# Kernel optimization log

Hardware: AMD Instinct MI355X
Metric: run time of the kernel (lower is better)

The kernel has to match this reference:

```python
import jax, jax.numpy as jnp
import numpy as np

HIDDEN = 4096
MOE_INTER = 1024
SHARED_INTER = 4096  # intermediate_size * num_shared_expert
NUM_EXPERTS = 16
TOP_K = 2


def setup_inputs() -> dict:
    key = jax.random.key(0)
    ks = jax.random.split(key, 6)
    s = 0.02
    hidden_states = jax.random.normal(ks[0], (2, 2048, HIDDEN), dtype=jnp.float32)
    gate_w = jax.random.normal(ks[1], (NUM_EXPERTS, HIDDEN), dtype=jnp.float32) * s
    # per-expert SwiGLU weights: gate_up [E, 2I, H], down [E, H, I]
    w_gate_up = jax.random.normal(ks[2], (NUM_EXPERTS, 2 * MOE_INTER, HIDDEN), dtype=jnp.float32) * s
    w_down = jax.random.normal(ks[3], (NUM_EXPERTS, HIDDEN, MOE_INTER), dtype=jnp.float32) * s
    shared_w_gate_up = jax.random.normal(ks[4], (2 * SHARED_INTER, HIDDEN), dtype=jnp.float32) * s
    shared_w_down = jax.random.normal(ks[5], (HIDDEN, SHARED_INTER), dtype=jnp.float32) * s
    return {
        'hidden_states': hidden_states,
        'gate_w': gate_w,
        'w_gate_up': w_gate_up,
        'w_down': w_down,
        'shared_w_gate_up': shared_w_gate_up,
        'shared_w_down': shared_w_down,
    }


def _moe_forward(x, gate_w, w_gate_up, w_down, shared_w_gate_up, shared_w_down):
    orig_shape = x.shape
    x2 = x.reshape(-1, orig_shape[-1])  # [T, H]

    # shared SwiGLU MLP (reduce_results=False in TP; single device here)
    gu_s = x2 @ shared_w_gate_up.T  # [T, 2*Is]
    g_s, u_s = jnp.split(gu_s, 2, axis=-1)
    shared_out = (jax.nn.silu(g_s) * u_s) @ shared_w_down.T  # [T, H]

    # router: softmax -> top-k -> renormalize (top_k > 1)
    logits = x2 @ gate_w.T  # [T, E]
    probs = jax.nn.softmax(logits, axis=-1)
    topk_vals, topk_idx = jax.lax.top_k(probs, TOP_K)  # [T, K]
    topk_vals = topk_vals / jnp.sum(topk_vals, axis=-1, keepdims=True)
    # combine weights [T, E]: sparse top-k weights scattered into dense matrix
    combine = jnp.sum(
        jax.nn.one_hot(topk_idx, NUM_EXPERTS, dtype=x2.dtype) * topk_vals[..., None],
        axis=1,
    )

    # dense per-expert SwiGLU (reference for fused grouped-GEMM)
    gu = jnp.einsum('th,eih->eti', x2, w_gate_up)  # [E, T, 2I]
    g, u = jnp.split(gu, 2, axis=-1)
    act = jax.nn.silu(g) * u  # [E, T, I]
    out_e = jnp.einsum('eti,ehi->eth', act, w_down)  # [E, T, H]
    moe_out = jnp.einsum('eth,te->th', out_e, combine)  # [T, H]

    return (moe_out + shared_out).reshape(orig_shape)


def reference(hidden_states, gate_w, w_gate_up, w_down, shared_w_gate_up, shared_w_down):
    return _moe_forward(hidden_states, gate_w, w_gate_up, w_down,
                        shared_w_gate_up, shared_w_down)
```

## Files before the change

### kernel.cpp

```cpp
#include <hip/hip_runtime.h>
#include <hip/hip_bf16.h>

#define H 4096
#define MOE_I 1024
#define SH_I 4096
#define NE 16
#define T_TOK 4096
#define NPAIR 8192

using bf16x8 = __attribute__((ext_vector_type(8))) short;
using f32x4  = __attribute__((ext_vector_type(4))) float;

__device__ __forceinline__ unsigned short f2bf(float f) {
    unsigned int x = __float_as_uint(f);
    x += 0x7fffu + ((x >> 16) & 1u);
    return (unsigned short)(x >> 16);
}
__device__ __forceinline__ float bf2f(unsigned short u) {
    return __uint_as_float(((unsigned int)u) << 16);
}

__device__ __forceinline__ void gld_lds16(const void* g, void* l) {
    __builtin_amdgcn_global_load_lds(
        (const __attribute__((address_space(1))) void*)g,
        (__attribute__((address_space(3))) void*)l, 16, 0, 0);
}

__global__ __launch_bounds__(256)
void cast_kernel(const float4* __restrict__ src, ushort4* __restrict__ dst, int n4) {
    int i = blockIdx.x * 256 + threadIdx.x;
    if (i < n4) {
        float4 f = src[i];
        ushort4 o;
        o.x = f2bf(f.x); o.y = f2bf(f.y); o.z = f2bf(f.z); o.w = f2bf(f.w);
        dst[i] = o;
    }
}

__global__ __launch_bounds__(256)
void router_kernel(const float* __restrict__ x, const float* __restrict__ gw,
                   int* __restrict__ topk_id, float* __restrict__ topk_w,
                   int* __restrict__ counts) {
    int t = blockIdx.x;
    const float* xr = x + (size_t)t * H;
    __shared__ float lg[NE];
    int tid = threadIdx.x, w = tid >> 6, lane = tid & 63;
#pragma unroll
    for (int i = 0; i < 4; i++) {
        int e = w * 4 + i;
        const float* g = gw + (size_t)e * H;
        float s = 0.f;
        for (int k = lane; k < H; k += 64) s += xr[k] * g[k];
#pragma unroll
        for (int m = 32; m > 0; m >>= 1) s += __shfl_xor(s, m, 64);
        if (lane == 0) lg[e] = s;
    }
    __syncthreads();
    if (tid == 0) {
        int e0 = 0; float l0 = lg[0];
        for (int e = 1; e < NE; e++) if (lg[e] > l0) { l0 = lg[e]; e0 = e; }
        int e1 = -1; float l1 = -1e30f;
        for (int e = 0; e < NE; e++) if (e != e0 && lg[e] > l1) { l1 = lg[e]; e1 = e; }
        float w1 = 1.f / (1.f + __expf(l0 - l1));
        topk_id[2*t] = e0; topk_id[2*t+1] = e1;
        topk_w[2*t] = 1.f - w1; topk_w[2*t+1] = w1;
        atomicAdd(&counts[e0], 1); atomicAdd(&counts[e1], 1);
    }
}

__global__ void scan16(const int* __restrict__ counts, int* __restrict__ offsets,
                       int* __restrict__ cursor) {
    if (threadIdx.x == 0 && blockIdx.x == 0) {
        int s = 0;
        for (int e = 0; e < NE; e++) { offsets[e] = s; cursor[e] = s; s += counts[e]; }
        offsets[NE] = s;
    }
}

__global__ __launch_bounds__(256)
void assign_kernel(const int* __restrict__ topk_id, const float* __restrict__ topk_w,
                   int* __restrict__ cursor, int* __restrict__ perm_tok,
                   float* __restrict__ perm_w) {
    int t = blockIdx.x * blockDim.x + threadIdx.x;
    if (t >= T_TOK) return;
    for (int k = 0; k < 2; k++) {
        int e = topk_id[2*t+k];
        int pos = atomicAdd(&cursor[e], 1);
        perm_tok[pos] = t;
        perm_w[pos] = topk_w[2*t+k];
    }
}

template<int MODE>
__global__ __launch_bounds__(256)
void gemm_tile(const unsigned short* __restrict__ A0,
               const unsigned short* __restrict__ B0,
               unsigned short* __restrict__ Cb,
               float* __restrict__ Cf,
               const int* __restrict__ offsets,
               const int* __restrict__ perm_tok,
               const float* __restrict__ perm_w,
               int K, int N, int M, int ldc) {
    int e = 0, off = 0, cnt = M;
    if constexpr (MODE >= 2) {
        e = blockIdx.z;
        off = offsets[e];
        cnt = offsets[e + 1] - off;
    }
    const int m0 = blockIdx.y * 128, n0 = blockIdx.x * 128;
    if (m0 >= cnt) return;

    __shared__ __align__(16) unsigned short lds_a[128 * 32];
    __shared__ __align__(16) unsigned short lds_b[128 * 32];

    const int tid = threadIdx.x, w = tid >> 6, lane = tid & 63;
    const unsigned short* B = B0 + (size_t)e * N * K;

    const unsigned short* aptr[2];
    const unsigned short* bptr[2];
    unsigned short* la[2];
    unsigned short* lb[2];
#pragma unroll
    for (int j = 0; j < 2; j++) {
        int c = w * 2 + j;
        int r = m0 + ((c * 64 + lane) >> 2);
        int rcl = (r < cnt - 1) ? r : (cnt - 1);
        int rs;
        if constexpr (MODE == 2)      rs = perm_tok[off + rcl];
        else if constexpr (MODE == 3) rs = off + rcl;
        else                          rs = r;
        aptr[j] = A0 + (size_t)rs * K + (lane & 3) * 8;
        int rn = n0 + ((c * 64 + lane) >> 2);
        bptr[j] = B + (size_t)rn * K + (lane & 3) * 8;
        la[j] = &lds_a[c * 512];
        lb[j] = &lds_b[c * 512];
    }

    f32x4 acc[4][4];
#pragma unroll
    for (int i = 0; i < 4; i++)
#pragma unroll
        for (int j = 0; j < 4; j++) acc[i][j] = (f32x4){0.f, 0.f, 0.f, 0.f};

    const int wm = (w & 1) * 64, wn = (w >> 1) * 64;
    const int quad = lane >> 4, r16 = lane & 15;

    for (int k0 = 0; k0 < K; k0 += 32) {
        gld_lds16(aptr[0], la[0]);
        gld_lds16(aptr[1], la[1]);
        gld_lds16(bptr[0], lb[0]);
        gld_lds16(bptr[1], lb[1]);
        aptr[0] += 32; aptr[1] += 32; bptr[0] += 32; bptr[1] += 32;
        __syncthreads();
        bf16x8 af[4], bfr[4];
#pragma unroll
        for (int mi = 0; mi < 4; mi++)
            af[mi] = *(const bf16x8*)&lds_a[(wm + mi * 16 + r16) * 32 + quad * 8];
#pragma unroll
        for (int ni = 0; ni < 4; ni++)
            bfr[ni] = *(const bf16x8*)&lds_b[(wn + ni * 16 + r16) * 32 + quad * 8];
#pragma unroll
        for (int mi = 0; mi < 4; mi++)
#pragma unroll
            for (int ni = 0; ni < 4; ni++)
                acc[mi][ni] = __builtin_amdgcn_mfma_f32_16x16x32_bf16(
                    af[mi], bfr[ni], acc[mi][ni], 0, 0, 0);
        __syncthreads();
    }

#pragma unroll
    for (int mi = 0; mi < 4; mi++) {
#pragma unroll
        for (int ni = 0; ni < 4; ni++) {
            f32x4 v = acc[mi][ni];
            int col = n0 + wn + ni * 16 + r16;
#pragma unroll
            for (int r = 0; r < 4; r++) {
                int row = m0 + wm + mi * 16 + quad * 4 + r;
                if (row < cnt) {
                    if constexpr (MODE == 0)
                        Cb[(size_t)row * ldc + col] = f2bf(v[r]);
                    else if constexpr (MODE == 1)
                        Cf[(size_t)row * ldc + col] = v[r];
                    else if constexpr (MODE == 2)
                        Cb[(size_t)(off + row) * ldc + col] = f2bf(v[r]);
                    else {
                        int tok = perm_tok[off + row];
                        float wt = perm_w[off + row];
                        atomicAdd(&Cf[(size_t)tok * ldc + col], wt * v[r]);
                    }
                }
            }
        }
    }
}

template<int SHIFT>
__global__ __launch_bounds__(256)
void swiglu_kernel(const unsigned short* __restrict__ gu, unsigned short* __restrict__ act,
                   long long total) {
    long long idx = ((long long)blockIdx.x * 256 + threadIdx.x) * 8;
    if (idx >= total) return;
    const int half = 1 << SHIFT;
    long long row = idx >> SHIFT;
    int cb = (int)(idx & (half - 1));
    const unsigned short* gp = gu + (row << (SHIFT + 1)) + cb;
    bf16x8 g8 = *(const bf16x8*)gp;
    bf16x8 u8 = *(const bf16x8*)(gp + half);
    bf16x8 res;
#pragma unroll
    for (int i = 0; i < 8; i++) {
        float g = bf2f((unsigned short)g8[i]);
        float u = bf2f((unsigned short)u8[i]);
        float a = g / (1.f + __expf(-g));
        res[i] = (short)f2bf(a * u);
    }
    *(bf16x8*)(act + idx) = res;
}

extern "C" void kernel_launch(void* const* d_in, const int* in_sizes, int n_in,
                              void* d_out, int out_size, void* d_ws, size_t ws_size,
                              hipStream_t stream) {
    const float* x         = (const float*)d_in[0];
    const float* gate_w    = (const float*)d_in[1];
    const float* w_gate_up = (const float*)d_in[2];
    const float* w_down    = (const float*)d_in[3];
    const float* s_wgu     = (const float*)d_in[4];
    const float* s_wd      = (const float*)d_in[5];
    float* out = (float*)d_out;

    char* p = (char*)d_ws;
    auto alloc = [&](size_t bytes) {
        char* q = p;
        p += (bytes + 255) & ~(size_t)255;
        return q;
    };
    unsigned short* x_bf    = (unsigned short*)alloc((size_t)T_TOK * H * 2);
    unsigned short* wgu_bf  = (unsigned short*)alloc((size_t)NE * 2 * MOE_I * H * 2);
    unsigned short* wd_bf   = (unsigned short*)alloc((size_t)NE * H * MOE_I * 2);
    unsigned short* swgu_bf = (unsigned short*)alloc((size_t)2 * SH_I * H * 2);
    unsigned short* swd_bf  = (unsigned short*)alloc((size_t)H * SH_I * 2);
    unsigned short* gu_s    = (unsigned short*)alloc((size_t)T_TOK * 2 * SH_I * 2);
    unsigned short* act_s   = (unsigned short*)alloc((size_t)T_TOK * SH_I * 2);
    unsigned short* gu_e    = (unsigned short*)alloc((size_t)NPAIR * 2 * MOE_I * 2);
    unsigned short* act_e   = (unsigned short*)alloc((size_t)NPAIR * MOE_I * 2);
    int*   topk_id  = (int*)alloc(T_TOK * 2 * 4);
    float* topk_w   = (float*)alloc(T_TOK * 2 * 4);
    int*   counts   = (int*)alloc(NE * 4);
    int*   offsets  = (int*)alloc((NE + 1) * 4);
    int*   cursor   = (int*)alloc(NE * 4);
    int*   perm_tok = (int*)alloc(NPAIR * 4);
    float* perm_w   = (float*)alloc(NPAIR * 4);

    hipMemsetAsync(counts, 0, 768, stream);

    auto cast = [&](const float* s, unsigned short* d, size_t n) {
        int n4 = (int)(n / 4);
        cast_kernel<<<(n4 + 255) / 256, 256, 0, stream>>>((const float4*)s, (ushort4*)d, n4);
    };
    cast(x, x_bf, (size_t)T_TOK * H);
    cast(w_gate_up, wgu_bf, (size_t)NE * 2 * MOE_I * H);
    cast(w_down, wd_bf, (size_t)NE * H * MOE_I);
    cast(s_wgu, swgu_bf, (size_t)2 * SH_I * H);
    cast(s_wd, swd_bf, (size_t)H * SH_I);

    router_kernel<<<T_TOK, 256, 0, stream>>>(x, gate_w, topk_id, topk_w, counts);
    scan16<<<1, 64, 0, stream>>>(counts, offsets, cursor);
    assign_kernel<<<16, 256, 0, stream>>>(topk_id, topk_w, cursor, perm_tok, perm_w);

    gemm_tile<0><<<dim3(2 * SH_I / 128, T_TOK / 128, 1), 256, 0, stream>>>(
        x_bf, swgu_bf, gu_s, nullptr, nullptr, nullptr, nullptr, H, 2 * SH_I, T_TOK, 2 * SH_I);
    swiglu_kernel<12><<<(int)(((long long)T_TOK * SH_I / 8 + 255) / 256), 256, 0, stream>>>(
        gu_s, act_s, (long long)T_TOK * SH_I);
    gemm_tile<1><<<dim3(H / 128, T_TOK / 128, 1), 256, 0, stream>>>(
        act_s, swd_bf, nullptr, out, nullptr, nullptr, nullptr, SH_I, H, T_TOK, H);

    gemm_tile<2><<<dim3(2 * MOE_I / 128, T_TOK / 128, NE), 256, 0, stream>>>(
        x_bf, wgu_bf, gu_e, nullptr, offsets, perm_tok, nullptr, H, 2 * MOE_I, 0, 2 * MOE_I);
    swiglu_kernel<10><<<(int)(((long long)NPAIR * MOE_I / 8 + 255) / 256), 256, 0, stream>>>(
        gu_e, act_e, (long long)NPAIR * MOE_I);
    gemm_tile<3><<<dim3(H / 128, T_TOK / 128, NE), 256, 0, stream>>>(
        act_e, wd_bf, nullptr, out, offsets, perm_tok, perm_w, MOE_I, H, 0, H);
}
```

Before: 2.447 ms.

## Replace 128x128 GEMM with double-buffered 256x256 swizzled-LDS MFMA kernel

Replaces the GEMM kernel used by all four matmuls. The old kernel used 128x128 tiles, 256 threads and a single LDS buffer synchronised on both sides of each k-step. The new one uses 256x256 tiles with 512 threads (8 waves) and a 128KB dynamic LDS double buffer over a 64-wide k tile. Global-to-LDS loads for the next stage are issued in the middle of the current MFMA work, with an XOR swizzle against LDS bank conflicts and s_setprio around the MFMA bursts. The goal is more data reuse per tile and overlap of memory and compute. The cost is higher register and LDS pressure (one block per CU) and more wasted work on partially filled expert tiles.

```diff
diff --git a/kernel.cpp b/kernel.cpp
--- a/kernel.cpp
+++ b/kernel.cpp
@@ -92,103 +92,170 @@
 }
 
 template<int MODE>
-__global__ __launch_bounds__(256)
-void gemm_tile(const unsigned short* __restrict__ A0,
-               const unsigned short* __restrict__ B0,
-               unsigned short* __restrict__ Cb,
-               float* __restrict__ Cf,
-               const int* __restrict__ offsets,
-               const int* __restrict__ perm_tok,
-               const float* __restrict__ perm_w,
-               int K, int N, int M, int ldc) {
+__global__ __launch_bounds__(512, 2)
+void gemm8(const unsigned short* __restrict__ A0,
+           const unsigned short* __restrict__ B0,
+           unsigned short* __restrict__ Cb, float* __restrict__ Cf,
+           const int* __restrict__ offsets, const int* __restrict__ perm_tok,
+           const float* __restrict__ perm_w,
+           int K, int N, int M, int ldc) {
+    extern __shared__ char smem[];
     int e = 0, off = 0, cnt = M;
-    if constexpr (MODE >= 2) {
-        e = blockIdx.z;
-        off = offsets[e];
-        cnt = offsets[e + 1] - off;
-    }
-    const int m0 = blockIdx.y * 128, n0 = blockIdx.x * 128;
+    if constexpr (MODE >= 2) { e = blockIdx.z; off = offsets[e]; cnt = offsets[e + 1] - off; }
+    const int m0 = blockIdx.y * 256, n0 = blockIdx.x * 256;
     if (m0 >= cnt) return;
-
-    __shared__ __align__(16) unsigned short lds_a[128 * 32];
-    __shared__ __align__(16) unsigned short lds_b[128 * 32];
+    const unsigned short* Bp = B0 + (size_t)e * N * K;
 
     const int tid = threadIdx.x, w = tid >> 6, lane = tid & 63;
-    const unsigned short* B = B0 + (size_t)e * N * K;
-
-    const unsigned short* aptr[2];
-    const unsigned short* bptr[2];
-    unsigned short* la[2];
-    unsigned short* lb[2];
-#pragma unroll
-    for (int j = 0; j < 2; j++) {
-        int c = w * 2 + j;
-        int r = m0 + ((c * 64 + lane) >> 2);
-        int rcl = (r < cnt - 1) ? r : (cnt - 1);
-        int rs;
-        if constexpr (MODE == 2)      rs = perm_tok[off + rcl];
-        else if constexpr (MODE == 3) rs = off + rcl;
-        else                          rs = r;
-        aptr[j] = A0 + (size_t)rs * K + (lane & 3) * 8;
-        int rn = n0 + ((c * 64 + lane) >> 2);
-        bptr[j] = B + (size_t)rn * K + (lane & 3) * 8;
-        la[j] = &lds_a[c * 512];
-        lb[j] = &lds_b[c * 512];
-    }
-
-    f32x4 acc[4][4];
-#pragma unroll
-    for (int i = 0; i < 4; i++)
+    const int wr = w >> 2, wc = w & 3;
+    const int quad = lane >> 4, r16 = lane & 15;
+
+    const unsigned short* srcA[2][2];
+    const unsigned short* srcB[2][2];
+    int dstA[2][2], dstB[2][2];
+#pragma unroll
+    for (int kh = 0; kh < 2; kh++)
+#pragma unroll
+        for (int j = 0; j < 2; j++) {
+            int D  = (j * 8 + w) * 1024 + lane * 16;
+            int r  = D >> 6;
+            int sl = (D >> 4) & 3;
+            int sg = sl ^ ((r >> 1) & 3);
+            int ra = m0 + r; if (ra > cnt - 1) ra = cnt - 1;
+            int rs;
+            if constexpr (MODE == 2)      rs = perm_tok[off + ra];
+            else if constexpr (MODE == 3) rs = off + ra;
+            else                          rs = ra;
+            srcA[kh][j] = A0 + (size_t)rs * K + kh * 32 + sg * 8;
+            srcB[kh][j] = Bp + (size_t)(n0 + r) * K + kh * 32 + sg * 8;
+            dstA[kh][j] = kh * 16384 + (j * 8 + w) * 1024;
+            dstB[kh][j] = 32768 + dstA[kh][j];
+        }
+
+    const int swz  = (quad ^ ((r16 >> 1) & 3)) * 16;
+    const int aoff = (wr * 128 + r16) * 64 + swz;
+    const int boff = 32768 + (wc * 64 + r16) * 64 + swz;
+
+    f32x4 acc[8][4];
+#pragma unroll
+    for (int i = 0; i < 8; i++)
 #pragma unroll
         for (int j = 0; j < 4; j++) acc[i][j] = (f32x4){0.f, 0.f, 0.f, 0.f};
 
-    const int wm = (w & 1) * 64, wn = (w >> 1) * 64;
-    const int quad = lane >> 4, r16 = lane & 15;
-
-    for (int k0 = 0; k0 < K; k0 += 32) {
-        gld_lds16(aptr[0], la[0]);
-        gld_lds16(aptr[1], la[1]);
-        gld_lds16(bptr[0], lb[0]);
-        gld_lds16(bptr[1], lb[1]);
-        aptr[0] += 32; aptr[1] += 32; bptr[0] += 32; bptr[1] += 32;
-        __syncthreads();
-        bf16x8 af[4], bfr[4];
-#pragma unroll
-        for (int mi = 0; mi < 4; mi++)
-            af[mi] = *(const bf16x8*)&lds_a[(wm + mi * 16 + r16) * 32 + quad * 8];
-#pragma unroll
-        for (int ni = 0; ni < 4; ni++)
-            bfr[ni] = *(const bf16x8*)&lds_b[(wn + ni * 16 + r16) * 32 + quad * 8];
+    const int nt = K >> 6;
+
+#pragma unroll
+    for (int kh = 0; kh < 2; kh++) {
+        gld_lds16(srcA[kh][0], smem + dstA[kh][0]);
+        gld_lds16(srcA[kh][1], smem + dstA[kh][1]);
+        gld_lds16(srcB[kh][0], smem + dstB[kh][0]);
+        gld_lds16(srcB[kh][1], smem + dstB[kh][1]);
+    }
+    {
+        int adv0 = (nt > 1) ? 64 : 0;
+#pragma unroll
+        for (int kh = 0; kh < 2; kh++)
+#pragma unroll
+            for (int j = 0; j < 2; j++) { srcA[kh][j] += adv0; srcB[kh][j] += adv0; }
+    }
+
+    for (int t = 0; t < nt; t++) {
+        char* sb = smem + (t & 1) * 65536;
+        char* so = smem + ((t + 1) & 1) * 65536;
+        const int adv = (t + 2 < nt) ? 64 : 0;
+        bf16x8 av[4], bv[4];
+
+        asm volatile("s_waitcnt vmcnt(4)" ::: "memory");
+        __builtin_amdgcn_s_barrier();
+        asm volatile("" ::: "memory");
+        gld_lds16(srcA[0][0], so + dstA[0][0]);
+        gld_lds16(srcA[0][1], so + dstA[0][1]);
+        srcA[0][0] += adv; srcA[0][1] += adv;
+#pragma unroll
+        for (int mi = 0; mi < 4; mi++) av[mi] = *(const bf16x8*)(sb + mi * 1024 + aoff);
+#pragma unroll
+        for (int ni = 0; ni < 4; ni++) bv[ni] = *(const bf16x8*)(sb + ni * 1024 + boff);
+        __builtin_amdgcn_s_setprio(1);
 #pragma unroll
         for (int mi = 0; mi < 4; mi++)
 #pragma unroll
             for (int ni = 0; ni < 4; ni++)
                 acc[mi][ni] = __builtin_amdgcn_mfma_f32_16x16x32_bf16(
-                    af[mi], bfr[ni], acc[mi][ni], 0, 0, 0);
-        __syncthreads();
-    }
-
-#pragma unroll
-    for (int mi = 0; mi < 4; mi++) {
-#pragma unroll
-        for (int ni = 0; ni < 4; ni++) {
-            f32x4 v = acc[mi][ni];
-            int col = n0 + wn + ni * 16 + r16;
-#pragma unroll
-            for (int r = 0; r < 4; r++) {
-                int row = m0 + wm + mi * 16 + quad * 4 + r;
-                if (row < cnt) {
+                    av[mi], bv[ni], acc[mi][ni], 0, 0, 0);
+        __builtin_amdgcn_s_setprio(0);
+        gld_lds16(srcB[0][0], so + dstB[0][0]);
+        gld_lds16(srcB[0][1], so + dstB[0][1]);
+        srcB[0][0] += adv; srcB[0][1] += adv;
+#pragma unroll
+        for (int mi = 0; mi < 4; mi++) av[mi] = *(const bf16x8*)(sb + (mi + 4) * 1024 + aoff);
+        __builtin_amdgcn_s_setprio(1);
+#pragma unroll
+        for (int mi = 0; mi < 4; mi++)
+#pragma unroll
+            for (int ni = 0; ni < 4; ni++)
+                acc[mi + 4][ni] = __builtin_amdgcn_mfma_f32_16x16x32_bf16(
+                    av[mi], bv[ni], acc[mi + 4][ni], 0, 0, 0);
+        __builtin_amdgcn_s_setprio(0);
+
+        asm volatile("s_waitcnt vmcnt(4)" ::: "memory");
+        __builtin_amdgcn_s_barrier();
+        asm volatile("" ::: "memory");
+        gld_lds16(srcA[1][0], so + dstA[1][0]);
+        gld_lds16(srcA[1][1], so + dstA[1][1]);
+        srcA[1][0] += adv; srcA[1][1] += adv;
+#pragma unroll
+        for (int mi = 0; mi < 4; mi++) av[mi] = *(const bf16x8*)(sb + 16384 + mi * 1024 + aoff);
+#pragma unroll
+        for (int ni = 0; ni < 4; ni++) bv[ni] = *(const bf16x8*)(sb + 16384 + ni * 1024 + boff);
+        __builtin_amdgcn_s_setprio(1);
+#pragma unroll
+        for (int mi = 0; mi < 4; mi++)
+#pragma unroll
+            for (int ni = 0; ni < 4; ni++)
+                acc[mi][ni] = __builtin_amdgcn_mfma_f32_16x16x32_bf16(
+                    av[mi], bv[ni], acc[mi][ni], 0, 0, 0);
+        __builtin_amdgcn_s_setprio(0);
+        gld_lds16(srcB[1][0], so + dstB[1][0]);
+        gld_lds16(srcB[1][1], so + dstB[1][1]);
+        srcB[1][0] += adv; srcB[1][1] += adv;
+#pragma unroll
+        for (int mi = 0; mi < 4; mi++) av[mi] = *(const bf16x8*)(sb + 16384 + (mi + 4) * 1024 + aoff);
+        __builtin_amdgcn_s_setprio(1);
+#pragma unroll
+        for (int mi = 0; mi < 4; mi++)
+#pragma unroll
+            for (int ni = 0; ni < 4; ni++)
+                acc[mi + 4][ni] = __builtin_amdgcn_mfma_f32_16x16x32_bf16(
+                    av[mi], bv[ni], acc[mi + 4][ni], 0, 0, 0);
+        __builtin_amdgcn_s_setprio(0);
+    }
+
+    asm volatile("s_waitcnt vmcnt(0)" ::: "memory");
+
+    const int rowlim = cnt - m0;
+#pragma unroll
+    for (int mi = 0; mi < 8; mi++) {
+#pragma unroll
+        for (int rr = 0; rr < 4; rr++) {
+            int r = wr * 128 + mi * 16 + quad * 4 + rr;
+            if (r < rowlim) {
+                int tok = 0; float wt = 0.f;
+                if constexpr (MODE == 3) {
+                    tok = perm_tok[off + m0 + r];
+                    wt  = perm_w[off + m0 + r];
+                }
+#pragma unroll
+                for (int ni = 0; ni < 4; ni++) {
+                    int col = n0 + wc * 64 + ni * 16 + r16;
+                    float v = acc[mi][ni][rr];
                     if constexpr (MODE == 0)
-                        Cb[(size_t)row * ldc + col] = f2bf(v[r]);
+                        Cb[(size_t)(m0 + r) * ldc + col] = f2bf(v);
                     else if constexpr (MODE == 1)
-                        Cf[(size_t)row * ldc + col] = v[r];
+                        Cf[(size_t)(m0 + r) * ldc + col] = v;
                     else if constexpr (MODE == 2)
-                        Cb[(size_t)(off + row) * ldc + col] = f2bf(v[r]);
-                    else {
-                        int tok = perm_tok[off + row];
-                        float wt = perm_w[off + row];
-                        atomicAdd(&Cf[(size_t)tok * ldc + col], wt * v[r]);
-                    }
+                        Cb[(size_t)(off + m0 + r) * ldc + col] = f2bf(v);
+                    else
+                        atomicAdd(&Cf[(size_t)tok * ldc + col], wt * v);
                 }
             }
         }
@@ -254,6 +321,16 @@
 
     hipMemsetAsync(counts, 0, 768, stream);
 
+    const int SHMEM = 131072;
+    static int attr_done = 0;
+    if (!attr_done) {
+        hipFuncSetAttribute((const void*)gemm8<0>, hipFuncAttributeMaxDynamicSharedMemorySize, SHMEM);
+        hipFuncSetAttribute((const void*)gemm8<1>, hipFuncAttributeMaxDynamicSharedMemorySize, SHMEM);
+        hipFuncSetAttribute((const void*)gemm8<2>, hipFuncAttributeMaxDynamicSharedMemorySize, SHMEM);
+        hipFuncSetAttribute((const void*)gemm8<3>, hipFuncAttributeMaxDynamicSharedMemorySize, SHMEM);
+        attr_done = 1;
+    }
+
     auto cast = [&](const float* s, unsigned short* d, size_t n) {
         int n4 = (int)(n / 4);
         cast_kernel<<<(n4 + 255) / 256, 256, 0, stream>>>((const float4*)s, (ushort4*)d, n4);
@@ -268,17 +345,17 @@
     scan16<<<1, 64, 0, stream>>>(counts, offsets, cursor);
     assign_kernel<<<16, 256, 0, stream>>>(topk_id, topk_w, cursor, perm_tok, perm_w);
 
-    gemm_tile<0><<<dim3(2 * SH_I / 128, T_TOK / 128, 1), 256, 0, stream>>>(
+    gemm8<0><<<dim3(2 * SH_I / 256, T_TOK / 256, 1), 512, SHMEM, stream>>>(
         x_bf, swgu_bf, gu_s, nullptr, nullptr, nullptr, nullptr, H, 2 * SH_I, T_TOK, 2 * SH_I);
     swiglu_kernel<12><<<(int)(((long long)T_TOK * SH_I / 8 + 255) / 256), 256, 0, stream>>>(
         gu_s, act_s, (long long)T_TOK * SH_I);
-    gemm_tile<1><<<dim3(H / 128, T_TOK / 128, 1), 256, 0, stream>>>(
+    gemm8<1><<<dim3(H / 256, T_TOK / 256, 1), 512, SHMEM, stream>>>(
         act_s, swd_bf, nullptr, out, nullptr, nullptr, nullptr, SH_I, H, T_TOK, H);
 
-    gemm_tile<2><<<dim3(2 * MOE_I / 128, T_TOK / 128, NE), 256, 0, stream>>>(
+    gemm8<2><<<dim3(2 * MOE_I / 256, T_TOK / 256, NE), 512, SHMEM, stream>>>(
         x_bf, wgu_bf, gu_e, nullptr, offsets, perm_tok, nullptr, H, 2 * MOE_I, 0, 2 * MOE_I);
     swiglu_kernel<10><<<(int)(((long long)NPAIR * MOE_I / 8 + 255) / 256), 256, 0, stream>>>(
         gu_e, act_e, (long long)NPAIR * MOE_I);
-    gemm_tile<3><<<dim3(H / 128, T_TOK / 128, NE), 256, 0, stream>>>(
+    gemm8<3><<<dim3(H / 256, T_TOK / 256, NE), 512, SHMEM, stream>>>(
         act_e, wd_bf, nullptr, out, offsets, perm_tok, perm_w, MOE_I, H, 0, H);
 }
```

Measured after the change: 2.073 ms. 1.18x faster.
